# Kernel optimization log

Measured on AMD Instinct MI355X. Metric: run time of the kernel, lower is better.

Reference implementation:

```python
import jax, jax.numpy as jnp
import numpy as np

B, T, S = 64, 32, 64          # batch, decoder steps, encoder memory length
V, E, H = 32000, 512, 1024    # vocab, emb_dim, hid_st_dim (= attention units/layer size)


def setup_inputs() -> dict:
    key = jax.random.key(0)
    ks = jax.random.split(key, 20)
    p = lambda k, shp, s=0.05: (jax.random.normal(k, shp, dtype=jnp.float32) * s)
    return {
        "tokens": jax.random.randint(ks[0], (B, T), 0, V),
        "memory": jax.random.normal(ks[1], (B, S, H), dtype=jnp.float32),
        "enc_h": jax.random.normal(ks[2], (B, H), dtype=jnp.float32),
        "enc_c": jax.random.normal(ks[3], (B, H), dtype=jnp.float32),
        "emb": p(ks[4], (V, E), 0.02),
        # layer-0 LSTM: input = concat(embedded token, prev attention) -> E + H
        "k0": p(ks[5], (E + H, 4 * H)), "r0": p(ks[6], (H, 4 * H)), "b0": jnp.zeros((4 * H,), jnp.float32),
        # layer-1 LSTM: input = layer-0 hidden
        "k1": p(ks[7], (H, 4 * H)), "r1": p(ks[8], (H, 4 * H)), "b1": jnp.zeros((4 * H,), jnp.float32),
        # Bahdanau attention: query/memory layers (no bias) + score vector v
        "Wq": p(ks[9], (H, H)), "Wk": p(ks[10], (H, H)), "v": p(ks[11], (H,)),
        # attention_layer: Dense(H, use_bias=False) on concat(cell_out, context)
        "Wa": p(ks[12], (2 * H, H)),
        # output projection to vocab
        "Wfc": p(ks[13], (H, V)), "bfc": jnp.zeros((V,), jnp.float32),
    }


def _lstm(x, h, c, K, R, b):
    z = x @ K + h @ R + b
    i, f, g, o = jnp.split(z, 4, axis=-1)  # TF gate order: i, f, g(c), o
    c = jax.nn.sigmoid(f) * c + jax.nn.sigmoid(i) * jnp.tanh(g)
    h = jax.nn.sigmoid(o) * jnp.tanh(c)
    return h, c


def reference(tokens, memory, enc_h, enc_c, emb, k0, r0, b0, k1, r1, b1,
              Wq, Wk, v, Wa, Wfc, bfc):
    x = emb[tokens]                      # [B, T, E] teacher-forced inputs
    keys = memory @ Wk                   # [B, S, H] precomputed memory projection

    def step(carry, x_t):
        h0, c0, h1, c1, attn = carry
        cell_in = jnp.concatenate([x_t, attn], axis=-1)       # AttentionWrapper input
        h0, c0 = _lstm(cell_in, h0, c0, k0, r0, b0)
        h1, c1 = _lstm(h0, h1, c1, k1, r1, b1)
        q = h1 @ Wq                                           # [B, H]
        score = jnp.einsum('u,bsu->bs', v, jnp.tanh(keys + q[:, None, :]))
        align = jax.nn.softmax(score, axis=-1)                # full-length memory: no mask
        ctx = jnp.einsum('bs,bsm->bm', align, memory)         # [B, H]
        attn = jnp.concatenate([h1, ctx], axis=-1) @ Wa       # attention_layer output
        return (h0, c0, h1, c1, attn), attn                   # output_attention=True

    init = (enc_h, enc_c, enc_h, enc_c, jnp.zeros((B, H), x.dtype))
    _, outs = jax.lax.scan(step, init, jnp.swapaxes(x, 0, 1))  # [T, B, H]
    outs = jnp.swapaxes(outs, 0, 1)                            # [B, T, H]
    logits = outs @ Wfc + bfc                                  # [B, T, V]
    return logits
```

## Files before the change

### kernel.cpp

```cpp
#include <hip/hip_runtime.h>
#include <math.h>


#define Bsz 64
#define Tsz 32
#define Ssz 64
#define Vsz 32000
#define Esz 512
#define Hsz 1024

__device__ __forceinline__ float sigm(float x) { return 1.0f / (1.0f + __expf(-x)); }

template <int BM, int BN, int TM, int TN>
__global__ __launch_bounds__(256) void gemm_t(
    const float* __restrict__ A, const float* __restrict__ W,
    const float* __restrict__ bias, const int* __restrict__ gather,
    float* __restrict__ C, int M, int N, int K, int lda)
{
    static_assert(BM == 128 && TN == 8, "cfg");
    constexpr int THRN = BN / TN;
    __shared__ float As[16][BM];
    __shared__ float Bs[16][BN];

    const int t  = threadIdx.x;
    const int bm = blockIdx.x * BM;
    const int bn = blockIdx.y * BN;
    const int tx = t % THRN;
    const int ty = t / THRN;

    float acc[TM][TN];
#pragma unroll
    for (int i = 0; i < TM; ++i)
#pragma unroll
        for (int j = 0; j < TN; ++j) acc[i][j] = 0.0f;

    const int am = t >> 1;
    const int ak = (t & 1) * 8;
    const int arow = gather ? gather[bm + am] : (bm + am);
    const float* Ap = A + (size_t)arow * lda + ak;

    for (int k0 = 0; k0 < K; k0 += 16) {
        float4 a0 = *(const float4*)(Ap + k0);
        float4 a1 = *(const float4*)(Ap + k0 + 4);
        As[ak + 0][am] = a0.x; As[ak + 1][am] = a0.y;
        As[ak + 2][am] = a0.z; As[ak + 3][am] = a0.w;
        As[ak + 4][am] = a1.x; As[ak + 5][am] = a1.y;
        As[ak + 6][am] = a1.z; As[ak + 7][am] = a1.w;
#pragma unroll
        for (int j = 0; j < BN / 64; ++j) {
            int flat = t + 256 * j;
            int kk = flat / (BN / 4);
            int n4 = (flat % (BN / 4)) * 4;
            *(float4*)&Bs[kk][n4] =
                *(const float4*)(W + (size_t)(k0 + kk) * N + bn + n4);
        }
        __syncthreads();
#pragma unroll
        for (int k = 0; k < 16; ++k) {
            float a[TM], b[TN];
#pragma unroll
            for (int i = 0; i < TM / 4; ++i)
                *(float4*)&a[i * 4] = *(const float4*)&As[k][ty * TM + i * 4];
            *(float4*)&b[0] = *(const float4*)&Bs[k][tx * 4];
            *(float4*)&b[4] = *(const float4*)&Bs[k][BN / 2 + tx * 4];
#pragma unroll
            for (int i = 0; i < TM; ++i)
#pragma unroll
                for (int j = 0; j < TN; ++j) acc[i][j] += a[i] * b[j];
        }
        __syncthreads();
    }

    float bv[8] = {0, 0, 0, 0, 0, 0, 0, 0};
    if (bias) {
#pragma unroll
        for (int j = 0; j < 4; ++j) {
            bv[j]     = bias[bn + tx * 4 + j];
            bv[4 + j] = bias[bn + BN / 2 + tx * 4 + j];
        }
    }
#pragma unroll
    for (int i = 0; i < TM; ++i) {
        int row = bm + ty * TM + i;
        float4 o0 = make_float4(acc[i][0] + bv[0], acc[i][1] + bv[1],
                                acc[i][2] + bv[2], acc[i][3] + bv[3]);
        float4 o1 = make_float4(acc[i][4] + bv[4], acc[i][5] + bv[5],
                                acc[i][6] + bv[6], acc[i][7] + bv[7]);
        *(float4*)(C + (size_t)row * N + bn + tx * 4) = o0;
        *(float4*)(C + (size_t)row * N + bn + BN / 2 + tx * 4) = o1;
    }
}

__global__ __launch_bounds__(256) void bgemm(
    const float* __restrict__ A1, int lda1,
    const float* __restrict__ A2, int lda2,
    const float* __restrict__ W1, const float* __restrict__ W2, int ldw,
    float* __restrict__ part, int Ntot, int p_off)
{
    __shared__ float As[16][64];
    __shared__ float Ws[16][256];

    const int t  = threadIdx.x;
    const int bn = blockIdx.x * 256;
    const int p  = blockIdx.y + p_off;

    const float* A; const float* W; int lda; int koff;
    if (p < 16) { A = A1; lda = lda1; W = W1; koff = p * 64; }
    else        { A = A2; lda = lda2; W = W2; koff = (p - 16) * 64; }

    const int tx = t & 31;
    const int ty = t >> 5;

    float acc[8][8];
#pragma unroll
    for (int i = 0; i < 8; ++i)
#pragma unroll
        for (int j = 0; j < 8; ++j) acc[i][j] = 0.0f;

    const int am = t >> 2;
    const int ak = (t & 3) * 4;
    const float* Ap = A + (size_t)am * lda + koff + ak;

    for (int kc = 0; kc < 64; kc += 16) {
        float4 av = *(const float4*)(Ap + kc);
        As[ak + 0][am] = av.x; As[ak + 1][am] = av.y;
        As[ak + 2][am] = av.z; As[ak + 3][am] = av.w;
#pragma unroll
        for (int j = 0; j < 4; ++j) {
            int flat = t + 256 * j;
            int kk = flat >> 6;
            int n4 = (flat & 63) * 4;
            *(float4*)&Ws[kk][n4] =
                *(const float4*)(W + (size_t)(koff + kc + kk) * ldw + bn + n4);
        }
        __syncthreads();
#pragma unroll
        for (int k = 0; k < 16; ++k) {
            float a[8], b[8];
            *(float4*)&a[0] = *(const float4*)&As[k][ty * 8];
            *(float4*)&a[4] = *(const float4*)&As[k][ty * 8 + 4];
            *(float4*)&b[0] = *(const float4*)&Ws[k][tx * 4];
            *(float4*)&b[4] = *(const float4*)&Ws[k][128 + tx * 4];
#pragma unroll
            for (int i = 0; i < 8; ++i)
#pragma unroll
                for (int j = 0; j < 8; ++j) acc[i][j] += a[i] * b[j];
        }
        __syncthreads();
    }

    float* outp = part + (size_t)p * 64 * Ntot + bn;
#pragma unroll
    for (int i = 0; i < 8; ++i) {
        int row = ty * 8 + i;
        *(float4*)(outp + (size_t)row * Ntot + tx * 4) =
            make_float4(acc[i][0], acc[i][1], acc[i][2], acc[i][3]);
        *(float4*)(outp + (size_t)row * Ntot + 128 + tx * 4) =
            make_float4(acc[i][4], acc[i][5], acc[i][6], acc[i][7]);
    }
}

__global__ __launch_bounds__(256) void lstm_k(
    const float* __restrict__ part, int pbase,
    const float* __restrict__ addin, int adstride,
    const float* __restrict__ bias,
    const float* __restrict__ cin, float* __restrict__ cout,
    float* __restrict__ hout)
{
    int idx = blockIdx.x * 256 + threadIdx.x;
    int b = idx >> 10;
    int h = idx & 1023;
    float zi = 0, zf = 0, zg = 0, zo = 0;
    for (int p = pbase; p < 32; ++p) {
        const float* q = part + (size_t)p * 64 * 4096 + b * 4096 + h;
        zi += q[0]; zf += q[1024]; zg += q[2048]; zo += q[3072];
    }
    if (addin) {
        const float* a = addin + (size_t)b * adstride + h;
        zi += a[0]; zf += a[1024]; zg += a[2048]; zo += a[3072];
    }
    if (bias) {
        zi += bias[h]; zf += bias[1024 + h];
        zg += bias[2048 + h]; zo += bias[3072 + h];
    }
    float cc = sigm(zf) * cin[idx] + sigm(zi) * tanhf(zg);
    cout[idx] = cc;
    hout[idx] = sigm(zo) * tanhf(cc);
}

__global__ __launch_bounds__(256) void attn_k(
    const float* __restrict__ qpart, const float* __restrict__ keys,
    const float* __restrict__ vvec, const float* __restrict__ mem,
    float* __restrict__ ctx)
{
    __shared__ float q_lds[1024];
    __shared__ float v_lds[1024];
    __shared__ float s_lds[64];
    const int b = blockIdx.x;
    const int t = threadIdx.x;

#pragma unroll
    for (int j = 0; j < 4; ++j) {
        int u = t + 256 * j;
        float acc = 0;
#pragma unroll
        for (int p = 0; p < 16; ++p) acc += qpart[(size_t)p * 65536 + b * 1024 + u];
        q_lds[u] = acc;
        v_lds[u] = vvec[u];
    }
    __syncthreads();

    const int s = t >> 2;
    const int uq = t & 3;
    const float* krow = keys + (size_t)b * (Ssz * Hsz) + s * Hsz;
    float sc = 0;
    for (int i = 0; i < 64; ++i) {
        int u = i * 16 + uq * 4;
        float4 kv = *(const float4*)(krow + u);
        sc += v_lds[u + 0] * tanhf(kv.x + q_lds[u + 0]);
        sc += v_lds[u + 1] * tanhf(kv.y + q_lds[u + 1]);
        sc += v_lds[u + 2] * tanhf(kv.z + q_lds[u + 2]);
        sc += v_lds[u + 3] * tanhf(kv.w + q_lds[u + 3]);
    }
    sc += __shfl_xor(sc, 1);
    sc += __shfl_xor(sc, 2);
    if (uq == 0) s_lds[s] = sc;
    __syncthreads();

    if (t < 64) {
        float x = s_lds[t];
        float mx = x;
        for (int d = 1; d < 64; d <<= 1) mx = fmaxf(mx, __shfl_xor(mx, d));
        float e = __expf(x - mx);
        float sm = e;
        for (int d = 1; d < 64; d <<= 1) sm += __shfl_xor(sm, d);
        s_lds[t] = e / sm;
    }
    __syncthreads();

#pragma unroll
    for (int j = 0; j < 4; ++j) {
        int m = t + 256 * j;
        float acc = 0;
        for (int s2 = 0; s2 < 64; ++s2)
            acc += s_lds[s2] * mem[(size_t)b * (Ssz * Hsz) + s2 * Hsz + m];
        ctx[b * 1024 + m] = acc;
    }
}

__global__ __launch_bounds__(256) void radd(
    const float* __restrict__ part, float* __restrict__ outs, int tstep)
{
    int idx = blockIdx.x * 256 + threadIdx.x;
    int b = idx >> 10;
    int n = idx & 1023;
    float acc = 0;
#pragma unroll
    for (int p = 0; p < 32; ++p) acc += part[(size_t)p * 65536 + idx];
    outs[((size_t)b * Tsz + tstep) * Hsz + n] = acc;
}

extern "C" void kernel_launch(void* const* d_in, const int* in_sizes, int n_in,
                              void* d_out, int out_size, void* d_ws, size_t ws_size,
                              hipStream_t stream)
{
    (void)in_sizes; (void)n_in; (void)out_size; (void)ws_size;
    const int*   tokens = (const int*)  d_in[0];
    const float* memory = (const float*)d_in[1];
    const float* enc_h  = (const float*)d_in[2];
    const float* enc_c  = (const float*)d_in[3];
    const float* emb    = (const float*)d_in[4];
    const float* k0     = (const float*)d_in[5];
    const float* r0     = (const float*)d_in[6];
    const float* b0     = (const float*)d_in[7];
    const float* k1     = (const float*)d_in[8];
    const float* r1     = (const float*)d_in[9];
    const float* b1     = (const float*)d_in[10];
    const float* Wq     = (const float*)d_in[11];
    const float* Wk     = (const float*)d_in[12];
    const float* vvec   = (const float*)d_in[13];
    const float* Wa     = (const float*)d_in[14];
    const float* Wfc    = (const float*)d_in[15];
    const float* bfc    = (const float*)d_in[16];
    float* out = (float*)d_out;

    float* w    = (float*)d_ws;
    float* xk   = w; w += (size_t)2048 * 4096;
    float* keys = w; w += (size_t)4096 * 1024;
    float* outs = w; w += (size_t)2048 * 1024;
    float* h0   = w; w += 65536;
    float* c0   = w; w += 65536;
    float* h1   = w; w += 65536;
    float* c1   = w; w += 65536;
    float* gp   = w; w += (size_t)32 * 64 * 4096;
    float* qp   = w; w += (size_t)16 * 65536;
    float* ap   = w; w += (size_t)32 * 65536;
    float* ctxb = w; w += 65536;

    gemm_t<128, 256, 16, 8><<<dim3(16, 16), 256, 0, stream>>>(
        emb, k0, b0, tokens, xk, 2048, 4096, Esz, Esz);
    gemm_t<128, 128, 8, 8><<<dim3(32, 8), 256, 0, stream>>>(
        memory, Wk, nullptr, nullptr, keys, 4096, 1024, 1024, 1024);

    const float* k0a = k0 + (size_t)Esz * 4096;

    for (int t = 0; t < Tsz; ++t) {
        const float* a_prev = outs + (size_t)(t - 1) * Hsz;
        const float* h0_in = (t == 0) ? enc_h : h0;
        const float* h1_in = (t == 0) ? enc_h : h1;
        const float* c0_in = (t == 0) ? enc_c : c0;
        const float* c1_in = (t == 0) ? enc_c : c1;

        if (t == 0)
            bgemm<<<dim3(16, 16), 256, 0, stream>>>(
                nullptr, 0, h0_in, 1024, k0a, r0, 4096, gp, 4096, 16);
        else
            bgemm<<<dim3(16, 32), 256, 0, stream>>>(
                a_prev, Tsz * Hsz, h0_in, 1024, k0a, r0, 4096, gp, 4096, 0);
        lstm_k<<<256, 256, 0, stream>>>(
            gp, (t == 0) ? 16 : 0, xk + (size_t)t * 4096, Tsz * 4096,
            nullptr, c0_in, c0, h0);
        bgemm<<<dim3(16, 32), 256, 0, stream>>>(
            h0, 1024, h1_in, 1024, k1, r1, 4096, gp, 4096, 0);
        lstm_k<<<256, 256, 0, stream>>>(
            gp, 0, nullptr, 0, b1, c1_in, c1, h1);
        bgemm<<<dim3(4, 16), 256, 0, stream>>>(
            h1, 1024, nullptr, 0, Wq, nullptr, 1024, qp, 1024, 0);
        attn_k<<<64, 256, 0, stream>>>(qp, keys, vvec, memory, ctxb);
        bgemm<<<dim3(4, 32), 256, 0, stream>>>(
            h1, 1024, ctxb, 1024, Wa, Wa + (size_t)1024 * 1024, 1024, ap, 1024, 0);
        radd<<<256, 256, 0, stream>>>(ap, outs, t);
    }

    gemm_t<128, 256, 16, 8><<<dim3(16, 125), 256, 0, stream>>>(
        outs, Wfc, bfc, nullptr, out, 2048, Vsz, 1024, 1024);
}
```

Baseline: 7.070 ms.

## Use split-bf16 MFMA for vocab projection and halve split-K partitions in recurrent GEMMs

Replaces the final FP32 SIMT GEMM onto the vocabulary with a bf16 MFMA kernel. Both operands are split into hi and lo bf16 parts and three cross products are accumulated to keep near-FP32 accuracy. Wfc is transposed and split in two halves into reused scratch space, and the attention outputs are split inside radd. Separately, the per-step bgemm split-K chunk grows from 64 to 128, halving the partial buffers and the reduction work in lstm_k, attn_k and radd, at the cost of fewer blocks per step launch.

```diff
diff --git a/kernel.cpp b/kernel.cpp
--- a/kernel.cpp
+++ b/kernel.cpp
@@ -1,4 +1,5 @@
 #include <hip/hip_runtime.h>
+#include <hip/hip_bf16.h>
 #include <math.h>
 
 
@@ -8,6 +9,9 @@
 #define Vsz 32000
 #define Esz 512
 #define Hsz 1024
+
+typedef short bhalf8 __attribute__((ext_vector_type(8)));
+typedef float floatx16 __attribute__((ext_vector_type(16)));
 
 __device__ __forceinline__ float sigm(float x) { return 1.0f / (1.0f + __expf(-x)); }
 
@@ -105,8 +109,8 @@
     const int p  = blockIdx.y + p_off;
 
     const float* A; const float* W; int lda; int koff;
-    if (p < 16) { A = A1; lda = lda1; W = W1; koff = p * 64; }
-    else        { A = A2; lda = lda2; W = W2; koff = (p - 16) * 64; }
+    if (p < 8) { A = A1; lda = lda1; W = W1; koff = p * 128; }
+    else       { A = A2; lda = lda2; W = W2; koff = (p - 8) * 128; }
 
     const int tx = t & 31;
     const int ty = t >> 5;
@@ -121,7 +125,7 @@
     const int ak = (t & 3) * 4;
     const float* Ap = A + (size_t)am * lda + koff + ak;
 
-    for (int kc = 0; kc < 64; kc += 16) {
+    for (int kc = 0; kc < 128; kc += 16) {
         float4 av = *(const float4*)(Ap + kc);
         As[ak + 0][am] = av.x; As[ak + 1][am] = av.y;
         As[ak + 2][am] = av.z; As[ak + 3][am] = av.w;
@@ -171,7 +175,7 @@
     int b = idx >> 10;
     int h = idx & 1023;
     float zi = 0, zf = 0, zg = 0, zo = 0;
-    for (int p = pbase; p < 32; ++p) {
+    for (int p = pbase; p < 16; ++p) {
         const float* q = part + (size_t)p * 64 * 4096 + b * 4096 + h;
         zi += q[0]; zf += q[1024]; zg += q[2048]; zo += q[3072];
     }
@@ -204,7 +208,7 @@
         int u = t + 256 * j;
         float acc = 0;
 #pragma unroll
-        for (int p = 0; p < 16; ++p) acc += qpart[(size_t)p * 65536 + b * 1024 + u];
+        for (int p = 0; p < 8; ++p) acc += qpart[(size_t)p * 65536 + b * 1024 + u];
         q_lds[u] = acc;
         v_lds[u] = vvec[u];
     }
@@ -249,15 +253,152 @@
 }
 
 __global__ __launch_bounds__(256) void radd(
-    const float* __restrict__ part, float* __restrict__ outs, int tstep)
+    const float* __restrict__ part, float* __restrict__ outs,
+    __hip_bfloat16* __restrict__ ahi, __hip_bfloat16* __restrict__ alo,
+    int tstep)
 {
     int idx = blockIdx.x * 256 + threadIdx.x;
     int b = idx >> 10;
     int n = idx & 1023;
     float acc = 0;
 #pragma unroll
-    for (int p = 0; p < 32; ++p) acc += part[(size_t)p * 65536 + idx];
-    outs[((size_t)b * Tsz + tstep) * Hsz + n] = acc;
+    for (int p = 0; p < 16; ++p) acc += part[(size_t)p * 65536 + idx];
+    size_t o = ((size_t)b * Tsz + tstep) * Hsz + n;
+    outs[o] = acc;
+    __hip_bfloat16 hi = __float2bfloat16(acc);
+    ahi[o] = hi;
+    alo[o] = __float2bfloat16(acc - __bfloat162float(hi));
+}
+
+__global__ __launch_bounds__(256) void splitT_k(
+    const float* __restrict__ Wfc, int colbase,
+    __hip_bfloat16* __restrict__ whiT, __hip_bfloat16* __restrict__ wloT)
+{
+    __shared__ float tile[64][65];
+    const int t  = threadIdx.x;
+    const int kt = blockIdx.x & 15;
+    const int nt = blockIdx.x >> 4;
+    const int kb = kt * 64;
+    const int nb = nt * 64;
+#pragma unroll
+    for (int it = 0; it < 16; ++it) {
+        int idx = it * 256 + t;
+        int r = idx >> 6, c = idx & 63;
+        tile[r][c] = Wfc[(size_t)(kb + r) * Vsz + colbase + nb + c];
+    }
+    __syncthreads();
+#pragma unroll
+    for (int it = 0; it < 16; ++it) {
+        int idx = it * 256 + t;
+        int r2 = idx >> 6, c2 = idx & 63;
+        float v = tile[c2][r2];
+        __hip_bfloat16 hi = __float2bfloat16(v);
+        __hip_bfloat16 lo = __float2bfloat16(v - __bfloat162float(hi));
+        size_t o = (size_t)(nb + r2) * 1024 + kb + c2;
+        whiT[o] = hi;
+        wloT[o] = lo;
+    }
+}
+
+__global__ __launch_bounds__(256) void mfmaC_k(
+    const __hip_bfloat16* __restrict__ ahi, const __hip_bfloat16* __restrict__ alo,
+    const __hip_bfloat16* __restrict__ whiT, const __hip_bfloat16* __restrict__ wloT,
+    const float* __restrict__ bfc, float* __restrict__ out, int colbase)
+{
+    __shared__ __align__(16) unsigned short smem[4 * 4096];
+
+    const int t    = threadIdx.x;
+    const int w    = t >> 6;
+    const int lane = t & 63;
+    const int mt = blockIdx.x & 15;
+    const int nt = blockIdx.x >> 4;
+    const int bm = mt * 128;
+    const int bn = nt * 128;
+
+    const int r16 = lane >> 2;
+    const int cp  = lane & 3;
+    const int rl0 = w * 32 + r16;
+    const int rl1 = rl0 + 16;
+    const int swst = (rl0 >> 1) & 3;
+    const int ps  = (cp ^ swst) * 8;
+    const size_t gA0 = (size_t)(bm + rl0) * 1024 + cp * 8;
+    const size_t gA1 = (size_t)(bm + rl1) * 1024 + cp * 8;
+    const size_t gW0 = (size_t)(bn + rl0) * 1024 + cp * 8;
+    const size_t gW1 = (size_t)(bn + rl1) * 1024 + cp * 8;
+    const int l0 = rl0 * 32 + ps;
+    const int l1 = rl1 * 32 + ps;
+
+    const int wm = w >> 1, wn = w & 1;
+    const int fr = lane & 31;
+    const int fh = lane >> 5;
+    const int swrd = (fr >> 1) & 3;
+    const int arow0 = (wm * 64 + fr) * 32;
+    const int arow1 = arow0 + 32 * 32;
+    const int nrow0 = (wn * 64 + fr) * 32;
+    const int nrow1 = nrow0 + 32 * 32;
+
+    floatx16 acc00 = {}, acc01 = {}, acc10 = {}, acc11 = {};
+
+    for (int k0 = 0; k0 < 1024; k0 += 32) {
+        bhalf8 vA0 = *(const bhalf8*)(ahi  + gA0 + k0);
+        bhalf8 vA1 = *(const bhalf8*)(ahi  + gA1 + k0);
+        bhalf8 vL0 = *(const bhalf8*)(alo  + gA0 + k0);
+        bhalf8 vL1 = *(const bhalf8*)(alo  + gA1 + k0);
+        bhalf8 vW0 = *(const bhalf8*)(whiT + gW0 + k0);
+        bhalf8 vW1 = *(const bhalf8*)(whiT + gW1 + k0);
+        bhalf8 vX0 = *(const bhalf8*)(wloT + gW0 + k0);
+        bhalf8 vX1 = *(const bhalf8*)(wloT + gW1 + k0);
+        *(bhalf8*)&smem[l0]          = vA0;
+        *(bhalf8*)&smem[l1]          = vA1;
+        *(bhalf8*)&smem[4096 + l0]   = vL0;
+        *(bhalf8*)&smem[4096 + l1]   = vL1;
+        *(bhalf8*)&smem[8192 + l0]   = vW0;
+        *(bhalf8*)&smem[8192 + l1]   = vW1;
+        *(bhalf8*)&smem[12288 + l0]  = vX0;
+        *(bhalf8*)&smem[12288 + l1]  = vX1;
+        __syncthreads();
+
+#pragma unroll
+        for (int kk = 0; kk < 2; ++kk) {
+            const int cpa = ((kk * 2 + fh) ^ swrd) * 8;
+            bhalf8 aH0 = *(const bhalf8*)&smem[arow0 + cpa];
+            bhalf8 aH1 = *(const bhalf8*)&smem[arow1 + cpa];
+            bhalf8 aL0 = *(const bhalf8*)&smem[4096 + arow0 + cpa];
+            bhalf8 aL1 = *(const bhalf8*)&smem[4096 + arow1 + cpa];
+            bhalf8 bH0 = *(const bhalf8*)&smem[8192 + nrow0 + cpa];
+            bhalf8 bH1 = *(const bhalf8*)&smem[8192 + nrow1 + cpa];
+            bhalf8 bL0 = *(const bhalf8*)&smem[12288 + nrow0 + cpa];
+            bhalf8 bL1 = *(const bhalf8*)&smem[12288 + nrow1 + cpa];
+
+            acc00 = __builtin_amdgcn_mfma_f32_32x32x16_bf16(aH0, bH0, acc00, 0, 0, 0);
+            acc01 = __builtin_amdgcn_mfma_f32_32x32x16_bf16(aH0, bH1, acc01, 0, 0, 0);
+            acc10 = __builtin_amdgcn_mfma_f32_32x32x16_bf16(aH1, bH0, acc10, 0, 0, 0);
+            acc11 = __builtin_amdgcn_mfma_f32_32x32x16_bf16(aH1, bH1, acc11, 0, 0, 0);
+            acc00 = __builtin_amdgcn_mfma_f32_32x32x16_bf16(aL0, bH0, acc00, 0, 0, 0);
+            acc01 = __builtin_amdgcn_mfma_f32_32x32x16_bf16(aL0, bH1, acc01, 0, 0, 0);
+            acc10 = __builtin_amdgcn_mfma_f32_32x32x16_bf16(aL1, bH0, acc10, 0, 0, 0);
+            acc11 = __builtin_amdgcn_mfma_f32_32x32x16_bf16(aL1, bH1, acc11, 0, 0, 0);
+            acc00 = __builtin_amdgcn_mfma_f32_32x32x16_bf16(aH0, bL0, acc00, 0, 0, 0);
+            acc01 = __builtin_amdgcn_mfma_f32_32x32x16_bf16(aH0, bL1, acc01, 0, 0, 0);
+            acc10 = __builtin_amdgcn_mfma_f32_32x32x16_bf16(aH1, bL0, acc10, 0, 0, 0);
+            acc11 = __builtin_amdgcn_mfma_f32_32x32x16_bf16(aH1, bL1, acc11, 0, 0, 0);
+        }
+        __syncthreads();
+    }
+
+    const int colg = colbase + bn + wn * 64 + fr;
+    const float bv0 = bfc[colg];
+    const float bv1 = bfc[colg + 32];
+#pragma unroll
+    for (int r = 0; r < 16; ++r) {
+        int rrow = (r & 3) + 8 * (r >> 2) + 4 * fh;
+        size_t row0 = (size_t)(bm + wm * 64 + rrow) * Vsz + colg;
+        size_t row1 = row0 + (size_t)32 * Vsz;
+        out[row0]      = acc00[r] + bv0;
+        out[row0 + 32] = acc01[r] + bv1;
+        out[row1]      = acc10[r] + bv0;
+        out[row1 + 32] = acc11[r] + bv1;
+    }
 }
 
 extern "C" void kernel_launch(void* const* d_in, const int* in_sizes, int n_in,
@@ -284,18 +425,24 @@
     const float* bfc    = (const float*)d_in[16];
     float* out = (float*)d_out;
 
-    float* w    = (float*)d_ws;
-    float* xk   = w; w += (size_t)2048 * 4096;
-    float* keys = w; w += (size_t)4096 * 1024;
-    float* outs = w; w += (size_t)2048 * 1024;
-    float* h0   = w; w += 65536;
-    float* c0   = w; w += 65536;
-    float* h1   = w; w += 65536;
-    float* c1   = w; w += 65536;
-    float* gp   = w; w += (size_t)32 * 64 * 4096;
-    float* qp   = w; w += (size_t)16 * 65536;
-    float* ap   = w; w += (size_t)32 * 65536;
-    float* ctxb = w; w += 65536;
+    char* wb = (char*)d_ws;
+    float* outs = (float*)wb; wb += (size_t)2048 * 1024 * 4;
+    float* h0   = (float*)wb; wb += 65536 * 4;
+    float* c0   = (float*)wb; wb += 65536 * 4;
+    float* h1   = (float*)wb; wb += 65536 * 4;
+    float* c1   = (float*)wb; wb += 65536 * 4;
+    float* ctxb = (float*)wb; wb += 65536 * 4;
+    __hip_bfloat16* ahi = (__hip_bfloat16*)wb; wb += (size_t)2048 * 1024 * 2;
+    __hip_bfloat16* alo = (__hip_bfloat16*)wb; wb += (size_t)2048 * 1024 * 2;
+
+    char* scr = wb;
+    float* xk   = (float*)scr;
+    float* keys = (float*)(scr + (size_t)2048 * 4096 * 4);
+    float* gp   = (float*)(scr + (size_t)(2048 * 4096 + 4096 * 1024) * 4);
+    float* qp   = (float*)(scr + (size_t)(2048 * 4096 + 4096 * 1024 + 16 * 64 * 4096) * 4);
+    float* ap   = (float*)(scr + (size_t)(2048 * 4096 + 4096 * 1024 + 16 * 64 * 4096 + 8 * 65536) * 4);
+    __hip_bfloat16* whiT = (__hip_bfloat16*)scr;
+    __hip_bfloat16* wloT = (__hip_bfloat16*)(scr + (size_t)16000 * 1024 * 2);
 
     gemm_t<128, 256, 16, 8><<<dim3(16, 16), 256, 0, stream>>>(
         emb, k0, b0, tokens, xk, 2048, 4096, Esz, Esz);
@@ -312,26 +459,28 @@
         const float* c1_in = (t == 0) ? enc_c : c1;
 
         if (t == 0)
+            bgemm<<<dim3(16, 8), 256, 0, stream>>>(
+                nullptr, 0, h0_in, 1024, k0a, r0, 4096, gp, 4096, 8);
+        else
             bgemm<<<dim3(16, 16), 256, 0, stream>>>(
-                nullptr, 0, h0_in, 1024, k0a, r0, 4096, gp, 4096, 16);
-        else
-            bgemm<<<dim3(16, 32), 256, 0, stream>>>(
                 a_prev, Tsz * Hsz, h0_in, 1024, k0a, r0, 4096, gp, 4096, 0);
         lstm_k<<<256, 256, 0, stream>>>(
-            gp, (t == 0) ? 16 : 0, xk + (size_t)t * 4096, Tsz * 4096,
+            gp, (t == 0) ? 8 : 0, xk + (size_t)t * 4096, Tsz * 4096,
             nullptr, c0_in, c0, h0);
-        bgemm<<<dim3(16, 32), 256, 0, stream>>>(
+        bgemm<<<dim3(16, 16), 256, 0, stream>>>(
             h0, 1024, h1_in, 1024, k1, r1, 4096, gp, 4096, 0);
         lstm_k<<<256, 256, 0, stream>>>(
             gp, 0, nullptr, 0, b1, c1_in, c1, h1);
-        bgemm<<<dim3(4, 16), 256, 0, stream>>>(
+        bgemm<<<dim3(4, 8), 256, 0, stream>>>(
             h1, 1024, nullptr, 0, Wq, nullptr, 1024, qp, 1024, 0);
         attn_k<<<64, 256, 0, stream>>>(qp, keys, vvec, memory, ctxb);
-        bgemm<<<dim3(4, 32), 256, 0, stream>>>(
+        bgemm<<<dim3(4, 16), 256, 0, stream>>>(
             h1, 1024, ctxb, 1024, Wa, Wa + (size_t)1024 * 1024, 1024, ap, 1024, 0);
-        radd<<<256, 256, 0, stream>>>(ap, outs, t);
-    }
-
-    gemm_t<128, 256, 16, 8><<<dim3(16, 125), 256, 0, stream>>>(
-        outs, Wfc, bfc, nullptr, out, 2048, Vsz, 1024, 1024);
-}
+        radd<<<256, 256, 0, stream>>>(ap, outs, ahi, alo, t);
+    }
+
+    for (int h = 0; h < 2; ++h) {
+        splitT_k<<<4000, 256, 0, stream>>>(Wfc, h * 16000, whiT, wloT);
+        mfmaC_k<<<2000, 256, 0, stream>>>(ahi, alo, whiT, wloT, bfc, out, h * 16000);
+    }
+}
```

Result: faster. 6.640 ms (-6.1%).
